# Performance work log

Hardware: AMD Instinct MI355X
Metric: run time of the kernel (lower is better)

The kernel has to match this reference:

```python
import jax, jax.numpy as jnp
import numpy as np

C = 256
CQK = C // 8  # query/key projection dim (in_dim // 8)
B, H, W = 4, 64, 64


def setup_inputs() -> dict:
    key = jax.random.key(0)
    ks = jax.random.split(key, 7)
    scale = 0.05
    x = jax.random.normal(ks[0], (B, C, H, W), dtype=jnp.float32)
    Wq = jax.random.normal(ks[1], (CQK, C), dtype=jnp.float32) * scale
    bq = jax.random.normal(ks[2], (CQK,), dtype=jnp.float32) * scale
    Wk = jax.random.normal(ks[3], (CQK, C), dtype=jnp.float32) * scale
    bk = jax.random.normal(ks[4], (CQK,), dtype=jnp.float32) * scale
    Wv = jax.random.normal(ks[5], (C, C), dtype=jnp.float32) * scale
    bv = jax.random.normal(ks[6], (C,), dtype=jnp.float32) * scale
    return {"x": x, "Wq": Wq, "bq": bq, "Wk": Wk, "bk": bk, "Wv": Wv, "bv": bv}


def reference(x, Wq, bq, Wk, bk, Wv, bv):
    b, c, h, w = x.shape
    n = h * w
    xf = x.reshape(b, c, n)  # [B, C, N]
    # 1x1 convs == per-pixel linear maps over channels
    q = jnp.einsum('dc,bcn->bnd', Wq, xf) + bq[None, None, :]   # [B, N, C/8]
    k = jnp.einsum('dc,bcn->bdn', Wk, xf) + bk[None, :, None]   # [B, C/8, N]
    v = jnp.einsum('dc,bcn->bdn', Wv, xf) + bv[None, :, None]   # [B, C, N]
    energy = jnp.einsum('bnd,bdm->bnm', q, k)                    # [B, N, N]
    attention = jax.nn.softmax(energy, axis=-1)                  # softmax over keys
    # out = V @ attention^T  (torch: bmm(proj_value, attention.permute(0,2,1)))
    out = jnp.einsum('bdm,bnm->bdn', v, attention)               # [B, C, N]
    return out.reshape(b, c, h, w) + x
```

## Files before the change

kernel.cpp:

```cpp
#include <hip/hip_runtime.h>
#include <math.h>

#define BATCH 4
#define CH    256
#define NPIX  4096
#define DQK   32

typedef short          s16;
typedef unsigned int   uint_t;
typedef __attribute__((ext_vector_type(8))) short short8;
typedef __attribute__((ext_vector_type(4))) float floatx4;
typedef __attribute__((ext_vector_type(16))) float floatx16;

__device__ __forceinline__ s16 f2bf(float f) {
  union { float f; uint_t u; } v; v.f = f;
  return (s16)((v.u + 0x8000u) >> 16);
}
__device__ __forceinline__ uint_t pk2(float a, float b) {
  union { float f; uint_t u; } x, y; x.f = a; y.f = b;
  return (((y.u + 0x8000u) >> 16) << 16) | ((x.u + 0x8000u) >> 16);
}

__global__ __launch_bounds__(256) void prepack(
    const float* __restrict__ Wq, const float* __restrict__ bq,
    const float* __restrict__ Wk, const float* __restrict__ bk,
    const float* __restrict__ Wv, const float* __restrict__ bv,
    s16* __restrict__ Wbf, float* __restrict__ Bsw)
{
  const int gid = blockIdx.x * 256 + threadIdx.x;
  const int e0  = gid * 4;
  const int row = e0 >> 8, col = e0 & 255;
  const float* src = (row < 32) ? Wq + (size_t)row * 256
                   : (row < 64) ? Wk + (size_t)(row - 32) * 256
                                : Wv + (size_t)(row - 64) * 256;
  float4 f = *(const float4*)(src + col);
  uint2 o; o.x = pk2(f.x, f.y); o.y = pk2(f.z, f.w);
  *(uint2*)(Wbf + e0) = o;
  if (gid < 320)
    Bsw[gid] = (gid < 32) ? bq[gid] : (gid < 64) ? bk[gid - 32] : bv[gid - 64];
}

__global__ __launch_bounds__(256, 2) void proj_mfma(
    const float* __restrict__ x, const s16* __restrict__ Wbf,
    const float* __restrict__ Bsw,
    s16* __restrict__ Qw, s16* __restrict__ Kw, s16* __restrict__ Vw)
{
  const int b  = blockIdx.x >> 7;
  const int n0 = (blockIdx.x & 127) << 5;
  const int t  = threadIdx.x;

  __shared__ s16 Xs[32][264];
  __shared__ s16 Os[256][40];

  const float* xb = x + (size_t)b * CH * NPIX + n0;
  #pragma unroll
  for (int i = 0; i < 2; ++i) {
    int task = i * 256 + t;
    int ncg  = task & 7;
    int kcg  = task >> 3;
    const float* src = xb + (size_t)(kcg * 4) * NPIX + ncg * 4;
    float rows[4][4];
    *(float4*)&rows[0][0] = *(const float4*)(src);
    *(float4*)&rows[1][0] = *(const float4*)(src + NPIX);
    *(float4*)&rows[2][0] = *(const float4*)(src + 2 * NPIX);
    *(float4*)&rows[3][0] = *(const float4*)(src + 3 * NPIX);
    #pragma unroll
    for (int c = 0; c < 4; ++c) {
      uint2 pk;
      pk.x = pk2(rows[0][c], rows[1][c]);
      pk.y = pk2(rows[2][c], rows[3][c]);
      *(uint2*)&Xs[ncg * 4 + c][kcg * 4] = pk;
    }
  }
  __syncthreads();

  const int w    = t >> 6;
  const int l15  = t & 15;
  const int quad = (t & 63) >> 4;

  floatx4 acc[5][2];
  #pragma unroll
  for (int si = 0; si < 5; ++si)
    #pragma unroll
    for (int nt = 0; nt < 2; ++nt) acc[si][nt] = (floatx4){0.f, 0.f, 0.f, 0.f};

  short8 afc[5], afn[5];
  #pragma unroll
  for (int si = 0; si < 5; ++si) {
    const int s = w + si * 4;
    afc[si] = *(const short8*)(Wbf + (size_t)(s * 16 + l15) * 256 + quad * 8);
  }
  for (int kc = 0; kc < 8; ++kc) {
    const int k0  = kc * 32;
    const int kn0 = (kc < 7) ? k0 + 32 : 0;
    #pragma unroll
    for (int si = 0; si < 5; ++si) {
      const int s = w + si * 4;
      afn[si] = *(const short8*)(Wbf + (size_t)(s * 16 + l15) * 256 + kn0 + quad * 8);
    }
    short8 bf[2];
    #pragma unroll
    for (int nt = 0; nt < 2; ++nt)
      bf[nt] = *(const short8*)&Xs[l15 + 16 * nt][k0 + quad * 8];
    #pragma unroll
    for (int si = 0; si < 5; ++si)
      #pragma unroll
      for (int nt = 0; nt < 2; ++nt)
        acc[si][nt] = __builtin_amdgcn_mfma_f32_16x16x32_bf16(afc[si], bf[nt], acc[si][nt], 0, 0, 0);
    #pragma unroll
    for (int si = 0; si < 5; ++si) afc[si] = afn[si];
  }

  #pragma unroll
  for (int si = 0; si < 5; ++si) {
    const int s = w + si * 4;
    float4 bb = *(const float4*)(Bsw + 16 * s + quad * 4);
    #pragma unroll
    for (int nt = 0; nt < 2; ++nt) {
      const int px  = 16 * nt + l15;
      float v0 = acc[si][nt][0] + bb.x;
      float v1 = acc[si][nt][1] + bb.y;
      float v2 = acc[si][nt][2] + bb.z;
      float v3 = acc[si][nt][3] + bb.w;
      if (s < 4) {
        s16* dst = (s < 2) ? Qw : Kw;
        int d0 = (s & 1) * 16 + quad * 4;
        uint2 pq; pq.x = pk2(v0, v1); pq.y = pk2(v2, v3);
        *(uint2*)(dst + ((size_t)b * NPIX + n0 + px) * DQK + d0) = pq;
      } else {
        const int c0 = (s - 4) * 16 + quad * 4;
        Os[c0 + 0][px] = f2bf(v0);
        Os[c0 + 1][px] = f2bf(v1);
        Os[c0 + 2][px] = f2bf(v2);
        Os[c0 + 3][px] = f2bf(v3);
      }
    }
  }
  __syncthreads();
  #pragma unroll
  for (int rep = 0; rep < 4; ++rep) {
    const int task = rep * 256 + t;
    const int fid  = task >> 6;
    const int ln   = task & 63;
    const int c    = fid >> 1;
    const int sl   = fid & 1;
    const int row  = c * 32 + (ln & 31);
    const int col  = sl * 16 + (ln >> 5) * 8;
    *(uint4*)(Vw + (((size_t)b * 8 + c) * 256 + (n0 >> 4) + sl) * 512 + ln * 8) =
        *(const uint4*)&Os[row][col];
  }
}

__global__ __launch_bounds__(1024, 4) void attn_mfma(
    const s16* __restrict__ Qw, const s16* __restrict__ Kw,
    const s16* __restrict__ Vt, const float* __restrict__ x,
    float* __restrict__ out)
{
  const int bi = blockIdx.x;
  const int b  = bi & 3;
  const int qt = bi >> 2;
  const int n0 = qt * 64;
  const int t  = threadIdx.x;
  const int w    = t >> 6;
  const int lane = t & 63;
  const int l15  = t & 15;
  const int quad = lane >> 4;
  const int l31  = t & 31;
  const int lh   = lane >> 5;
  const int l7   = t & 7;
  const int sw   = w & 7;
  const int sq   = w >> 3;
  const int c    = w & 7;
  const int kh   = w >> 3;

  __shared__ s16  Pt[2][64][128];
  __shared__ float Lsum[64][8];
  __shared__ float Ored[8][32][64];

  const s16* qbase = Qw + ((size_t)b * NPIX + n0 + sq * 32) * DQK;
  short8 qb[2];
  #pragma unroll
  for (int tq = 0; tq < 2; ++tq)
    qb[tq] = *(const short8*)(qbase + (size_t)(16 * tq + l15) * DQK + quad * 8);

  floatx16 o[2];
  #pragma unroll
  for (int i = 0; i < 16; ++i) { o[0][i] = 0.f; o[1][i] = 0.f; }
  float l_part[2] = {0.f, 0.f};

  const s16* kbase = Kw + (size_t)b * NPIX * DQK;
  const s16* vtb   = Vt + ((size_t)(b * 8 + c) * 256) * 512 + lane * 8;

  short8 ka_c, ka_n, va[4];
  ka_c = *(const short8*)(kbase + (size_t)(16 * sw + l15) * DQK + quad * 8);
  #pragma unroll
  for (int ks = 0; ks < 4; ++ks)
    va[ks] = *(const short8*)(vtb + (size_t)(ks + 4 * kh) * 512);

  int buf = 0;
  for (int kt = 0; kt < 32; ++kt) {
    const int m0  = kt * 128;
    const int mn0 = (kt < 31) ? m0 + 128 : 0;

    floatx4 sacc[2];
    #pragma unroll
    for (int tq = 0; tq < 2; ++tq)
      sacc[tq] = __builtin_amdgcn_mfma_f32_16x16x32_bf16(
                   ka_c, qb[tq], (floatx4){0.f, 0.f, 0.f, 0.f}, 0, 0, 0);

    ka_n = *(const short8*)(kbase + (size_t)(mn0 + 16 * sw + l15) * DQK + quad * 8);

    const int wslot = (((2 * sw + (quad >> 1)) ^ l7) << 3) + (quad & 1) * 4;
    #pragma unroll
    for (int tq = 0; tq < 2; ++tq) {
      float p0 = __expf(fminf(sacc[tq][0], 60.f));
      float p1 = __expf(fminf(sacc[tq][1], 60.f));
      float p2 = __expf(fminf(sacc[tq][2], 60.f));
      float p3 = __expf(fminf(sacc[tq][3], 60.f));
      l_part[tq] += (p0 + p1) + (p2 + p3);
      uint2 pk; pk.x = pk2(p0, p1); pk.y = pk2(p2, p3);
      *(uint2*)&Pt[buf][sq * 32 + 16 * tq + l15][wslot] = pk;
    }
    __syncthreads();

    #pragma unroll
    for (int ks = 0; ks < 4; ++ks) {
      const int rslot = ((2 * (ks + 4 * kh) + lh) ^ l7) << 3;
      short8 pb0 = *(const short8*)&Pt[buf][l31     ][rslot];
      short8 pb1 = *(const short8*)&Pt[buf][32 + l31][rslot];
      o[0] = __builtin_amdgcn_mfma_f32_32x32x16_bf16(va[ks], pb0, o[0], 0, 0, 0);
      o[1] = __builtin_amdgcn_mfma_f32_32x32x16_bf16(va[ks], pb1, o[1], 0, 0, 0);
    }
    const int sn = mn0 >> 4;
    #pragma unroll
    for (int ks = 0; ks < 4; ++ks)
      va[ks] = *(const short8*)(vtb + (size_t)(sn + ks + 4 * kh) * 512);

    ka_c = ka_n;
    buf ^= 1;
  }

  #pragma unroll
  for (int tq = 0; tq < 2; ++tq) {
    l_part[tq] += __shfl_xor(l_part[tq], 16);
    l_part[tq] += __shfl_xor(l_part[tq], 32);
  }
  if (quad == 0) {
    #pragma unroll
    for (int tq = 0; tq < 2; ++tq) Lsum[sq * 32 + 16 * tq + l15][sw] = l_part[tq];
  }
  if (kh == 1) {
    #pragma unroll
    for (int r = 0; r < 16; ++r) {
      const int chrow = (r & 3) + 8 * (r >> 2) + 4 * lh;
      Ored[c][chrow][l31]      = o[0][r];
      Ored[c][chrow][32 + l31] = o[1][r];
    }
  }
  __syncthreads();

  if (kh == 0) {
    const int q0 = l31, q1 = 32 + l31;
    float4 a0 = *(const float4*)&Lsum[q0][0];
    float4 a1 = *(const float4*)&Lsum[q0][4];
    float4 b0 = *(const float4*)&Lsum[q1][0];
    float4 b1 = *(const float4*)&Lsum[q1][4];
    float inv0 = 1.f / (((a0.x + a0.y) + (a0.z + a0.w)) +
                        ((a1.x + a1.y) + (a1.z + a1.w)));
    float inv1 = 1.f / (((b0.x + b0.y) + (b0.z + b0.w)) +
                        ((b1.x + b1.y) + (b1.z + b1.w)));
    #pragma unroll
    for (int r = 0; r < 16; ++r) {
      const int chrow = (r & 3) + 8 * (r >> 2) + 4 * lh;
      const int ch = c * 32 + chrow;
      const float s0 = o[0][r] + Ored[c][chrow][l31];
      const float s1 = o[1][r] + Ored[c][chrow][32 + l31];
      const size_t off0 = ((size_t)b * CH + ch) * NPIX + n0 + q0;
      const size_t off1 = ((size_t)b * CH + ch) * NPIX + n0 + q1;
      out[off0] = fmaf(s0, inv0, x[off0]);
      out[off1] = fmaf(s1, inv1, x[off1]);
    }
  }
}

extern "C" void kernel_launch(void* const* d_in, const int* in_sizes, int n_in,
                              void* d_out, int out_size, void* d_ws, size_t ws_size,
                              hipStream_t stream) {
  (void)in_sizes; (void)n_in; (void)out_size; (void)ws_size;
  const float* x  = (const float*)d_in[0];
  const float* Wq = (const float*)d_in[1];
  const float* bq = (const float*)d_in[2];
  const float* Wk = (const float*)d_in[3];
  const float* bk = (const float*)d_in[4];
  const float* Wv = (const float*)d_in[5];
  const float* bv = (const float*)d_in[6];
  float* out = (float*)d_out;

  unsigned char* ws = (unsigned char*)d_ws;
  s16*   Qw  = (s16*)ws;
  s16*   Kw  = (s16*)(ws + (size_t)1 * 1024 * 1024);
  s16*   Vt  = (s16*)(ws + (size_t)2 * 1024 * 1024);
  s16*   Wbf = (s16*)(ws + (size_t)10 * 1024 * 1024);
  float* Bsw = (float*)(ws + (size_t)10 * 1024 * 1024 + 256 * 1024);

  hipLaunchKernelGGL(prepack, dim3(80), dim3(256), 0, stream,
                     Wq, bq, Wk, bk, Wv, bv, Wbf, Bsw);
  hipLaunchKernelGGL(proj_mfma, dim3(512), dim3(256), 0, stream,
                     x, Wbf, Bsw, Qw, Kw, Vt);
  hipLaunchKernelGGL(attn_mfma, dim3(256), dim3(1024), 0, stream,
                     Qw, Kw, Vt, x, out);
}
```

Baseline: 139.3 us.

## Warp-specialize attention: score warps produce P, PV warps consume one tile behind

Splits the 16 waves into producer waves (8, computing QK^T scores and exp for all 64 queries) and consumer waves (8, each owning 32 channels and the full 128-key PV product). The consumers lag one tile behind through the double-buffered Pt. This removes the split-K partial-output reduction through the Ored shared buffer and lets score/exp work overlap with PV MFMAs across waves. The cost is load imbalance: the consumer waves do all PV MFMAs while the producer waves only do cheap score work, so the PV half could become the critical path.

```diff
diff --git a/kernel.cpp b/kernel.cpp
--- a/kernel.cpp
+++ b/kernel.cpp
@@ -168,98 +168,101 @@
   const int l31  = t & 31;
   const int lh   = lane >> 5;
   const int l7   = t & 7;
+  const bool is_s = (w < 8);
   const int sw   = w & 7;
-  const int sq   = w >> 3;
-  const int c    = w & 7;
-  const int kh   = w >> 3;
 
   __shared__ s16  Pt[2][64][128];
   __shared__ float Lsum[64][8];
-  __shared__ float Ored[8][32][64];
-
-  const s16* qbase = Qw + ((size_t)b * NPIX + n0 + sq * 32) * DQK;
-  short8 qb[2];
-  #pragma unroll
-  for (int tq = 0; tq < 2; ++tq)
-    qb[tq] = *(const short8*)(qbase + (size_t)(16 * tq + l15) * DQK + quad * 8);
-
+
+  const s16* kbase = Kw + (size_t)b * NPIX * DQK;
+  const s16* vtb   = Vt + ((size_t)(b * 8 + sw) * 256) * 512 + lane * 8;
+
+  short8 qb[4];
+  short8 ka_c;
+  float l_part[4] = {0.f, 0.f, 0.f, 0.f};
+  short8 va[8];
   floatx16 o[2];
   #pragma unroll
   for (int i = 0; i < 16; ++i) { o[0][i] = 0.f; o[1][i] = 0.f; }
-  float l_part[2] = {0.f, 0.f};
-
-  const s16* kbase = Kw + (size_t)b * NPIX * DQK;
-  const s16* vtb   = Vt + ((size_t)(b * 8 + c) * 256) * 512 + lane * 8;
-
-  short8 ka_c, ka_n, va[4];
-  ka_c = *(const short8*)(kbase + (size_t)(16 * sw + l15) * DQK + quad * 8);
-  #pragma unroll
-  for (int ks = 0; ks < 4; ++ks)
-    va[ks] = *(const short8*)(vtb + (size_t)(ks + 4 * kh) * 512);
-
-  int buf = 0;
+
+  if (is_s) {
+    const s16* qbase = Qw + ((size_t)b * NPIX + n0) * DQK;
+    #pragma unroll
+    for (int tq = 0; tq < 4; ++tq)
+      qb[tq] = *(const short8*)(qbase + (size_t)(16 * tq + l15) * DQK + quad * 8);
+    ka_c = *(const short8*)(kbase + (size_t)(16 * sw + l15) * DQK + quad * 8);
+  } else {
+    #pragma unroll
+    for (int ks = 0; ks < 8; ++ks)
+      va[ks] = *(const short8*)(vtb + (size_t)ks * 512);
+  }
+
+  const int wslot = (((2 * sw + (quad >> 1)) ^ l7) << 3) + (quad & 1) * 4;
+
   for (int kt = 0; kt < 32; ++kt) {
-    const int m0  = kt * 128;
-    const int mn0 = (kt < 31) ? m0 + 128 : 0;
-
-    floatx4 sacc[2];
-    #pragma unroll
-    for (int tq = 0; tq < 2; ++tq)
-      sacc[tq] = __builtin_amdgcn_mfma_f32_16x16x32_bf16(
-                   ka_c, qb[tq], (floatx4){0.f, 0.f, 0.f, 0.f}, 0, 0, 0);
-
-    ka_n = *(const short8*)(kbase + (size_t)(mn0 + 16 * sw + l15) * DQK + quad * 8);
-
-    const int wslot = (((2 * sw + (quad >> 1)) ^ l7) << 3) + (quad & 1) * 4;
-    #pragma unroll
-    for (int tq = 0; tq < 2; ++tq) {
-      float p0 = __expf(fminf(sacc[tq][0], 60.f));
-      float p1 = __expf(fminf(sacc[tq][1], 60.f));
-      float p2 = __expf(fminf(sacc[tq][2], 60.f));
-      float p3 = __expf(fminf(sacc[tq][3], 60.f));
-      l_part[tq] += (p0 + p1) + (p2 + p3);
-      uint2 pk; pk.x = pk2(p0, p1); pk.y = pk2(p2, p3);
-      *(uint2*)&Pt[buf][sq * 32 + 16 * tq + l15][wslot] = pk;
+    if (is_s) {
+      floatx4 sacc[4];
+      #pragma unroll
+      for (int tq = 0; tq < 4; ++tq)
+        sacc[tq] = __builtin_amdgcn_mfma_f32_16x16x32_bf16(
+                     ka_c, qb[tq], (floatx4){0.f, 0.f, 0.f, 0.f}, 0, 0, 0);
+
+      const int mn0 = (kt < 31) ? (kt + 1) * 128 : 0;
+      short8 ka_n = *(const short8*)(kbase +
+                      (size_t)(mn0 + 16 * sw + l15) * DQK + quad * 8);
+
+      #pragma unroll
+      for (int tq = 0; tq < 4; ++tq) {
+        float p0 = __expf(fminf(sacc[tq][0], 60.f));
+        float p1 = __expf(fminf(sacc[tq][1], 60.f));
+        float p2 = __expf(fminf(sacc[tq][2], 60.f));
+        float p3 = __expf(fminf(sacc[tq][3], 60.f));
+        l_part[tq] += (p0 + p1) + (p2 + p3);
+        uint2 pk; pk.x = pk2(p0, p1); pk.y = pk2(p2, p3);
+        *(uint2*)&Pt[kt & 1][16 * tq + l15][wslot] = pk;
+      }
+      ka_c = ka_n;
+    } else if (kt > 0) {
+      const int buf = (kt - 1) & 1;
+      #pragma unroll
+      for (int ks = 0; ks < 8; ++ks) {
+        const int rslot = ((2 * ks + lh) ^ l7) << 3;
+        short8 pb0 = *(const short8*)&Pt[buf][l31     ][rslot];
+        short8 pb1 = *(const short8*)&Pt[buf][32 + l31][rslot];
+        o[0] = __builtin_amdgcn_mfma_f32_32x32x16_bf16(va[ks], pb0, o[0], 0, 0, 0);
+        o[1] = __builtin_amdgcn_mfma_f32_32x32x16_bf16(va[ks], pb1, o[1], 0, 0, 0);
+      }
+      const int sn = kt * 8;
+      #pragma unroll
+      for (int ks = 0; ks < 8; ++ks)
+        va[ks] = *(const short8*)(vtb + (size_t)(sn + ks) * 512);
     }
     __syncthreads();
-
-    #pragma unroll
-    for (int ks = 0; ks < 4; ++ks) {
-      const int rslot = ((2 * (ks + 4 * kh) + lh) ^ l7) << 3;
-      short8 pb0 = *(const short8*)&Pt[buf][l31     ][rslot];
-      short8 pb1 = *(const short8*)&Pt[buf][32 + l31][rslot];
+  }
+
+  if (is_s) {
+    #pragma unroll
+    for (int tq = 0; tq < 4; ++tq) {
+      l_part[tq] += __shfl_xor(l_part[tq], 16);
+      l_part[tq] += __shfl_xor(l_part[tq], 32);
+    }
+    if (quad == 0) {
+      #pragma unroll
+      for (int tq = 0; tq < 4; ++tq) Lsum[16 * tq + l15][sw] = l_part[tq];
+    }
+  } else {
+    #pragma unroll
+    for (int ks = 0; ks < 8; ++ks) {
+      const int rslot = ((2 * ks + lh) ^ l7) << 3;
+      short8 pb0 = *(const short8*)&Pt[1][l31     ][rslot];
+      short8 pb1 = *(const short8*)&Pt[1][32 + l31][rslot];
       o[0] = __builtin_amdgcn_mfma_f32_32x32x16_bf16(va[ks], pb0, o[0], 0, 0, 0);
       o[1] = __builtin_amdgcn_mfma_f32_32x32x16_bf16(va[ks], pb1, o[1], 0, 0, 0);
     }
-    const int sn = mn0 >> 4;
-    #pragma unroll
-    for (int ks = 0; ks < 4; ++ks)
-      va[ks] = *(const short8*)(vtb + (size_t)(sn + ks + 4 * kh) * 512);
-
-    ka_c = ka_n;
-    buf ^= 1;
-  }
-
-  #pragma unroll
-  for (int tq = 0; tq < 2; ++tq) {
-    l_part[tq] += __shfl_xor(l_part[tq], 16);
-    l_part[tq] += __shfl_xor(l_part[tq], 32);
-  }
-  if (quad == 0) {
-    #pragma unroll
-    for (int tq = 0; tq < 2; ++tq) Lsum[sq * 32 + 16 * tq + l15][sw] = l_part[tq];
-  }
-  if (kh == 1) {
-    #pragma unroll
-    for (int r = 0; r < 16; ++r) {
-      const int chrow = (r & 3) + 8 * (r >> 2) + 4 * lh;
-      Ored[c][chrow][l31]      = o[0][r];
-      Ored[c][chrow][32 + l31] = o[1][r];
-    }
   }
   __syncthreads();
 
-  if (kh == 0) {
+  if (!is_s) {
     const int q0 = l31, q1 = 32 + l31;
     float4 a0 = *(const float4*)&Lsum[q0][0];
     float4 a1 = *(const float4*)&Lsum[q0][4];
@@ -272,13 +275,11 @@
     #pragma unroll
     for (int r = 0; r < 16; ++r) {
       const int chrow = (r & 3) + 8 * (r >> 2) + 4 * lh;
-      const int ch = c * 32 + chrow;
-      const float s0 = o[0][r] + Ored[c][chrow][l31];
-      const float s1 = o[1][r] + Ored[c][chrow][32 + l31];
+      const int ch = sw * 32 + chrow;
       const size_t off0 = ((size_t)b * CH + ch) * NPIX + n0 + q0;
       const size_t off1 = ((size_t)b * CH + ch) * NPIX + n0 + q1;
-      out[off0] = fmaf(s0, inv0, x[off0]);
-      out[off1] = fmaf(s1, inv1, x[off1]);
+      out[off0] = fmaf(o[0][r], inv0, x[off0]);
+      out[off1] = fmaf(o[1][r], inv1, x[off1]);
     }
   }
 }
```

After: 165.6 us. 18.9% more time.

## Software-pipeline QK^T/exp stage one tile ahead of PV MFMAs

Applied to the files above, without the earlier changes.

Restructures the main loop so each iteration computes the scores and exponentials for the next key tile into the alternate shared buffer, while the PV MFMAs run on the current tile. The P fragments are loaded into registers before the next tile's writes, and a single barrier sits at the end of each iteration. The PV MFMA block is wrapped in s_setprio to favour matrix issue. The goal is to overlap the exp/pack VALU work with the MFMA work. The cost is more register pressure from holding the pb fragments and a longer prologue.

```diff
diff --git a/kernel.cpp b/kernel.cpp
--- a/kernel.cpp
+++ b/kernel.cpp
@@ -170,8 +170,7 @@
   const int l7   = t & 7;
   const int sw   = w & 7;
   const int sq   = w >> 3;
-  const int c    = w & 7;
-  const int kh   = w >> 3;
+  const int kh   = sq;
 
   __shared__ s16  Pt[2][64][128];
   __shared__ float Lsum[64][8];
@@ -189,7 +188,7 @@
   float l_part[2] = {0.f, 0.f};
 
   const s16* kbase = Kw + (size_t)b * NPIX * DQK;
-  const s16* vtb   = Vt + ((size_t)(b * 8 + c) * 256) * 512 + lane * 8;
+  const s16* vtb   = Vt + ((size_t)(b * 8 + sw) * 256) * 512 + lane * 8;
 
   short8 ka_c, ka_n, va[4];
   ka_c = *(const short8*)(kbase + (size_t)(16 * sw + l15) * DQK + quad * 8);
@@ -197,20 +196,15 @@
   for (int ks = 0; ks < 4; ++ks)
     va[ks] = *(const short8*)(vtb + (size_t)(ks + 4 * kh) * 512);
 
-  int buf = 0;
-  for (int kt = 0; kt < 32; ++kt) {
-    const int m0  = kt * 128;
-    const int mn0 = (kt < 31) ? m0 + 128 : 0;
-
+  const int wslot = (((2 * sw + (quad >> 1)) ^ l7) << 3) + (quad & 1) * 4;
+
+  {
     floatx4 sacc[2];
     #pragma unroll
     for (int tq = 0; tq < 2; ++tq)
       sacc[tq] = __builtin_amdgcn_mfma_f32_16x16x32_bf16(
                    ka_c, qb[tq], (floatx4){0.f, 0.f, 0.f, 0.f}, 0, 0, 0);
-
-    ka_n = *(const short8*)(kbase + (size_t)(mn0 + 16 * sw + l15) * DQK + quad * 8);
-
-    const int wslot = (((2 * sw + (quad >> 1)) ^ l7) << 3) + (quad & 1) * 4;
+    ka_n = *(const short8*)(kbase + (size_t)(128 + 16 * sw + l15) * DQK + quad * 8);
     #pragma unroll
     for (int tq = 0; tq < 2; ++tq) {
       float p0 = __expf(fminf(sacc[tq][0], 60.f));
@@ -219,25 +213,58 @@
       float p3 = __expf(fminf(sacc[tq][3], 60.f));
       l_part[tq] += (p0 + p1) + (p2 + p3);
       uint2 pk; pk.x = pk2(p0, p1); pk.y = pk2(p2, p3);
-      *(uint2*)&Pt[buf][sq * 32 + 16 * tq + l15][wslot] = pk;
-    }
-    __syncthreads();
-
+      *(uint2*)&Pt[0][sq * 32 + 16 * tq + l15][wslot] = pk;
+    }
+    ka_c = ka_n;
+  }
+  __syncthreads();
+
+  for (int kt = 0; kt < 32; ++kt) {
+    const int buf = kt & 1;
+
+    short8 pb[4][2];
     #pragma unroll
     for (int ks = 0; ks < 4; ++ks) {
       const int rslot = ((2 * (ks + 4 * kh) + lh) ^ l7) << 3;
-      short8 pb0 = *(const short8*)&Pt[buf][l31     ][rslot];
-      short8 pb1 = *(const short8*)&Pt[buf][32 + l31][rslot];
-      o[0] = __builtin_amdgcn_mfma_f32_32x32x16_bf16(va[ks], pb0, o[0], 0, 0, 0);
-      o[1] = __builtin_amdgcn_mfma_f32_32x32x16_bf16(va[ks], pb1, o[1], 0, 0, 0);
-    }
-    const int sn = mn0 >> 4;
+      pb[ks][0] = *(const short8*)&Pt[buf][l31     ][rslot];
+      pb[ks][1] = *(const short8*)&Pt[buf][32 + l31][rslot];
+    }
+
+    if (kt < 31) {
+      floatx4 sacc[2];
+      #pragma unroll
+      for (int tq = 0; tq < 2; ++tq)
+        sacc[tq] = __builtin_amdgcn_mfma_f32_16x16x32_bf16(
+                     ka_c, qb[tq], (floatx4){0.f, 0.f, 0.f, 0.f}, 0, 0, 0);
+      const int mn2 = (kt < 30) ? (kt + 2) * 128 : 0;
+      ka_n = *(const short8*)(kbase + (size_t)(mn2 + 16 * sw + l15) * DQK + quad * 8);
+      #pragma unroll
+      for (int tq = 0; tq < 2; ++tq) {
+        float p0 = __expf(fminf(sacc[tq][0], 60.f));
+        float p1 = __expf(fminf(sacc[tq][1], 60.f));
+        float p2 = __expf(fminf(sacc[tq][2], 60.f));
+        float p3 = __expf(fminf(sacc[tq][3], 60.f));
+        l_part[tq] += (p0 + p1) + (p2 + p3);
+        uint2 pk; pk.x = pk2(p0, p1); pk.y = pk2(p2, p3);
+        *(uint2*)&Pt[buf ^ 1][sq * 32 + 16 * tq + l15][wslot] = pk;
+      }
+      ka_c = ka_n;
+    }
+
+    __builtin_amdgcn_s_setprio(1);
+    #pragma unroll
+    for (int ks = 0; ks < 4; ++ks) {
+      o[0] = __builtin_amdgcn_mfma_f32_32x32x16_bf16(va[ks], pb[ks][0], o[0], 0, 0, 0);
+      o[1] = __builtin_amdgcn_mfma_f32_32x32x16_bf16(va[ks], pb[ks][1], o[1], 0, 0, 0);
+    }
+    __builtin_amdgcn_s_setprio(0);
+
+    const int sn = ((kt + 1) & 31) * 8;
     #pragma unroll
     for (int ks = 0; ks < 4; ++ks)
       va[ks] = *(const short8*)(vtb + (size_t)(sn + ks + 4 * kh) * 512);
 
-    ka_c = ka_n;
-    buf ^= 1;
+    __syncthreads();
   }
 
   #pragma unroll
@@ -253,8 +280,8 @@
     #pragma unroll
     for (int r = 0; r < 16; ++r) {
       const int chrow = (r & 3) + 8 * (r >> 2) + 4 * lh;
-      Ored[c][chrow][l31]      = o[0][r];
-      Ored[c][chrow][32 + l31] = o[1][r];
+      Ored[sw][chrow][l31]      = o[0][r];
+      Ored[sw][chrow][32 + l31] = o[1][r];
     }
   }
   __syncthreads();
@@ -272,9 +299,9 @@
     #pragma unroll
     for (int r = 0; r < 16; ++r) {
       const int chrow = (r & 3) + 8 * (r >> 2) + 4 * lh;
-      const int ch = c * 32 + chrow;
-      const float s0 = o[0][r] + Ored[c][chrow][l31];
-      const float s1 = o[1][r] + Ored[c][chrow][32 + l31];
+      const int ch = sw * 32 + chrow;
+      const float s0 = o[0][r] + Ored[sw][chrow][l31];
+      const float s1 = o[1][r] + Ored[sw][chrow][32 + l31];
       const size_t off0 = ((size_t)b * CH + ch) * NPIX + n0 + q0;
       const size_t off1 = ((size_t)b * CH + ch) * NPIX + n0 + q1;
       out[off0] = fmaf(s0, inv0, x[off0]);
```

Measured after the change: 136.0 us. -2.3%, faster.
